# Kernel optimization log

Hardware: AMD Instinct MI355X
Metric: run time of the kernel (lower is better)

## Reference

```python
import jax, jax.numpy as jnp
import numpy as np

N, IN_FEATURES, OUT_FEATURES = 1048576, 32, 128


def setup_inputs() -> dict:
    key = jax.random.key(0)
    kx, kc = jax.random.split(key)
    x = jax.random.normal(kx, (N, IN_FEATURES), dtype=jnp.float32)
    # nn.init.normal_(centres, 0, 1); nn.init.constant_(log_sigmas, 0)
    centres = jax.random.normal(kc, (OUT_FEATURES, IN_FEATURES), dtype=jnp.float32)
    log_sigmas = jnp.zeros((OUT_FEATURES,), dtype=jnp.float32)
    return {"x": x, "centres": centres, "log_sigmas": log_sigmas}


def reference(x, centres, log_sigmas):
    x2 = jnp.sum(x * x, axis=-1, keepdims=True)            # (N, 1)
    c2 = jnp.sum(centres * centres, axis=-1)               # (out,)
    cross = jnp.einsum('ni,oi->no', x, centres)            # (N, out) GEMM
    sqdist = jnp.maximum(x2 - 2.0 * cross + c2, 0.0)       # clamp fp round-off
    # original: exp(-(sqrt(sqdist)/sigma)^2) == exp(-sqdist / sigma^2)
    inv_var = jnp.exp(-2.0 * log_sigmas)                   # (out,)
    return jnp.exp(-sqdist * inv_var)                      # (N, out)
```

## Files before the change

kernel.cpp:

```cpp
#include <hip/hip_runtime.h>

constexpr int IN_F   = 32;
constexpr int OUT_F  = 128;
constexpr int BLOCK  = 256;
constexpr int WAVES  = BLOCK / 64;
constexpr int RSTAGE = 8;

using f32x2  = __attribute__((ext_vector_type(2)))  float;
using f32x16 = __attribute__((ext_vector_type(16))) float;

__global__ __launch_bounds__(BLOCK, 4)
void rbf_kernel(const float* __restrict__ x,
                const float* __restrict__ centres,
                const float* __restrict__ log_sigmas,
                float* __restrict__ out,
                int rows_per_wave)
{
    __shared__ float4 xs[WAVES][RSTAGE][IN_F / 4];
    __shared__ float  x2s[WAVES][RSTAGE];

    const int tid  = threadIdx.x;
    const int wv   = tid >> 6;
    const int lane = tid & 63;

    const int o0 = lane * 2;
    const f32x16 c0lo = *reinterpret_cast<const f32x16*>(centres + (size_t)(o0 + 0) * IN_F);
    const f32x16 c0hi = *reinterpret_cast<const f32x16*>(centres + (size_t)(o0 + 0) * IN_F + 16);
    const f32x16 c1lo = *reinterpret_cast<const f32x16*>(centres + (size_t)(o0 + 1) * IN_F);
    const f32x16 c1hi = *reinterpret_cast<const f32x16*>(centres + (size_t)(o0 + 1) * IN_F + 16);

    float c2a = 0.f, c2b = 0.f;
    #pragma unroll
    for (int k = 0; k < 16; ++k) {
        c2a = fmaf(c0lo[k], c0lo[k], c2a);
        c2a = fmaf(c0hi[k], c0hi[k], c2a);
        c2b = fmaf(c1lo[k], c1lo[k], c2b);
        c2b = fmaf(c1hi[k], c1hi[k], c2b);
    }
    const float iv0 = __expf(-2.0f * log_sigmas[o0 + 0]);
    const float iv1 = __expf(-2.0f * log_sigmas[o0 + 1]);

    const size_t waveRow0 = ((size_t)blockIdx.x * WAVES + wv) * (size_t)rows_per_wave;
    const int rs = lane >> 3;
    const int q  = lane & 7;

    for (int it = 0; it < rows_per_wave; it += RSTAGE) {
        const float4 v = *reinterpret_cast<const float4*>(
            x + (waveRow0 + it) * IN_F + lane * 4);
        float s;
        s = v.x * v.x;
        s = fmaf(v.y, v.y, s);
        s = fmaf(v.z, v.z, s);
        s = fmaf(v.w, v.w, s);
        s += __shfl_xor(s, 1);
        s += __shfl_xor(s, 2);
        s += __shfl_xor(s, 4);
        xs[wv][rs][q] = v;
        if (q == 0) x2s[wv][rs] = s;
        __syncthreads();

        #pragma unroll
        for (int rr = 0; rr < RSTAGE; ++rr) {
            float acc0 = 0.f, acc1 = 0.f;
            #pragma unroll
            for (int u = 0; u < 4; ++u) {
                const float4 xq = xs[wv][rr][u];
                acc0 = fmaf(xq.x, c0lo[4*u+0], acc0);
                acc0 = fmaf(xq.y, c0lo[4*u+1], acc0);
                acc0 = fmaf(xq.z, c0lo[4*u+2], acc0);
                acc0 = fmaf(xq.w, c0lo[4*u+3], acc0);
                acc1 = fmaf(xq.x, c1lo[4*u+0], acc1);
                acc1 = fmaf(xq.y, c1lo[4*u+1], acc1);
                acc1 = fmaf(xq.z, c1lo[4*u+2], acc1);
                acc1 = fmaf(xq.w, c1lo[4*u+3], acc1);
            }
            #pragma unroll
            for (int u = 0; u < 4; ++u) {
                const float4 xq = xs[wv][rr][4 + u];
                acc0 = fmaf(xq.x, c0hi[4*u+0], acc0);
                acc0 = fmaf(xq.y, c0hi[4*u+1], acc0);
                acc0 = fmaf(xq.z, c0hi[4*u+2], acc0);
                acc0 = fmaf(xq.w, c0hi[4*u+3], acc0);
                acc1 = fmaf(xq.x, c1hi[4*u+0], acc1);
                acc1 = fmaf(xq.y, c1hi[4*u+1], acc1);
                acc1 = fmaf(xq.z, c1hi[4*u+2], acc1);
                acc1 = fmaf(xq.w, c1hi[4*u+3], acc1);
            }
            const float x2 = x2s[wv][rr];
            const float t0 = fmaxf(fmaf(-2.0f, acc0, x2 + c2a), 0.0f);
            const float t1 = fmaxf(fmaf(-2.0f, acc1, x2 + c2b), 0.0f);
            f32x2 o;
            o.x = __expf(-t0 * iv0);
            o.y = __expf(-t1 * iv1);
            __builtin_nontemporal_store(o,
                reinterpret_cast<f32x2*>(out + (waveRow0 + it + rr) * OUT_F + o0));
        }
        __syncthreads();
    }
}

extern "C" void kernel_launch(void* const* d_in, const int* in_sizes, int n_in,
                              void* d_out, int out_size, void* d_ws, size_t ws_size,
                              hipStream_t stream) {
    const float* x          = (const float*)d_in[0];
    const float* centres    = (const float*)d_in[1];
    const float* log_sigmas = (const float*)d_in[2];
    float* out = (float*)d_out;

    const int n = in_sizes[0] / IN_F;
    const int blocks = 2048;
    const int rows_per_block = n / blocks;
    const int rows_per_wave  = rows_per_block / WAVES;
    rbf_kernel<<<blocks, BLOCK, 0, stream>>>(x, centres, log_sigmas, out, rows_per_wave);
}
```

Before: 152.7 us.

## Split K across half-waves with permlane swap, packed FMA, and double-buffered staging

Each lane now computes four output columns over half of the input features, and partial sums from the two half-waves are combined with v_permlane32_swap. Dot products use packed two-wide FMAs, and outputs are written as float4 vectors. The x tile is staged in double-buffered LDS with a register prefetch two stages ahead, and block-wide barriers are replaced by a per-wave LDS waitcnt. The grid is doubled and output stores are no longer nontemporal, which could change cache behaviour on the large output write.

```diff
diff --git a/kernel.cpp b/kernel.cpp
--- a/kernel.cpp
+++ b/kernel.cpp
@@ -9,6 +9,10 @@
 using f32x2  = __attribute__((ext_vector_type(2)))  float;
 using f32x16 = __attribute__((ext_vector_type(16))) float;
 
+__device__ __forceinline__ void swap32(float& a, float& b) {
+    asm volatile("v_permlane32_swap_b32 %0, %1" : "+v"(a), "+v"(b));
+}
+
 __global__ __launch_bounds__(BLOCK, 4)
 void rbf_kernel(const float* __restrict__ x,
                 const float* __restrict__ centres,
@@ -16,86 +20,130 @@
                 float* __restrict__ out,
                 int rows_per_wave)
 {
-    __shared__ float4 xs[WAVES][RSTAGE][IN_F / 4];
-    __shared__ float  x2s[WAVES][RSTAGE];
+    __shared__ float4 xs[WAVES][2][RSTAGE][IN_F / 4];
+    __shared__ float  x2s[WAVES][2][RSTAGE];
 
     const int tid  = threadIdx.x;
     const int wv   = tid >> 6;
     const int lane = tid & 63;
+    const int j    = lane & 31;
+    const int h    = lane >> 5;
 
-    const int o0 = lane * 2;
-    const f32x16 c0lo = *reinterpret_cast<const f32x16*>(centres + (size_t)(o0 + 0) * IN_F);
-    const f32x16 c0hi = *reinterpret_cast<const f32x16*>(centres + (size_t)(o0 + 0) * IN_F + 16);
-    const f32x16 c1lo = *reinterpret_cast<const f32x16*>(centres + (size_t)(o0 + 1) * IN_F);
-    const f32x16 c1hi = *reinterpret_cast<const f32x16*>(centres + (size_t)(o0 + 1) * IN_F + 16);
+    const float* cb = centres + (size_t)(4 * j) * IN_F + 16 * h;
+    const f32x16 cA = *reinterpret_cast<const f32x16*>(cb + 0 * IN_F);
+    const f32x16 cB = *reinterpret_cast<const f32x16*>(cb + 1 * IN_F);
+    const f32x16 cC = *reinterpret_cast<const f32x16*>(cb + 2 * IN_F);
+    const f32x16 cD = *reinterpret_cast<const f32x16*>(cb + 3 * IN_F);
 
-    float c2a = 0.f, c2b = 0.f;
+    float q0 = 0.f, q1 = 0.f, q2 = 0.f, q3 = 0.f;
     #pragma unroll
     for (int k = 0; k < 16; ++k) {
-        c2a = fmaf(c0lo[k], c0lo[k], c2a);
-        c2a = fmaf(c0hi[k], c0hi[k], c2a);
-        c2b = fmaf(c1lo[k], c1lo[k], c2b);
-        c2b = fmaf(c1hi[k], c1hi[k], c2b);
+        q0 = fmaf(cA[k], cA[k], q0);
+        q1 = fmaf(cB[k], cB[k], q1);
+        q2 = fmaf(cC[k], cC[k], q2);
+        q3 = fmaf(cD[k], cD[k], q3);
     }
-    const float iv0 = __expf(-2.0f * log_sigmas[o0 + 0]);
-    const float iv1 = __expf(-2.0f * log_sigmas[o0 + 1]);
+    float ta, tb;
+    ta = q0; tb = q0; swap32(ta, tb); const float c20 = ta + tb;
+    ta = q1; tb = q1; swap32(ta, tb); const float c21 = ta + tb;
+    ta = q2; tb = q2; swap32(ta, tb); const float c22 = ta + tb;
+    ta = q3; tb = q3; swap32(ta, tb); const float c23 = ta + tb;
+
+    const float4 ls4 = *reinterpret_cast<const float4*>(log_sigmas + 4 * j);
+    const float iv0 = __expf(-2.0f * ls4.x);
+    const float iv1 = __expf(-2.0f * ls4.y);
+    const float iv2 = __expf(-2.0f * ls4.z);
+    const float iv3 = __expf(-2.0f * ls4.w);
 
     const size_t waveRow0 = ((size_t)blockIdx.x * WAVES + wv) * (size_t)rows_per_wave;
+    const float* xb = x   + waveRow0 * IN_F;
+    float*       ob = out + waveRow0 * OUT_F + 4 * j;
+
     const int rs = lane >> 3;
     const int q  = lane & 7;
+    const int nst = rows_per_wave / RSTAGE;
 
-    for (int it = 0; it < rows_per_wave; it += RSTAGE) {
-        const float4 v = *reinterpret_cast<const float4*>(
-            x + (waveRow0 + it) * IN_F + lane * 4);
-        float s;
-        s = v.x * v.x;
-        s = fmaf(v.y, v.y, s);
-        s = fmaf(v.z, v.z, s);
-        s = fmaf(v.w, v.w, s);
-        s += __shfl_xor(s, 1);
-        s += __shfl_xor(s, 2);
-        s += __shfl_xor(s, 4);
-        xs[wv][rs][q] = v;
-        if (q == 0) x2s[wv][rs] = s;
-        __syncthreads();
+    float4 vcur = *reinterpret_cast<const float4*>(xb + (size_t)rs * IN_F + q * 4);
+    float4 vnxt = *reinterpret_cast<const float4*>(xb + (size_t)(RSTAGE + rs) * IN_F + q * 4);
 
+    for (int s = 0; s < nst; ++s) {
+        const int buf = s & 1;
+
+        float ss = vcur.x * vcur.x;
+        ss = fmaf(vcur.y, vcur.y, ss);
+        ss = fmaf(vcur.z, vcur.z, ss);
+        ss = fmaf(vcur.w, vcur.w, ss);
+        ss += __shfl_xor(ss, 1);
+        ss += __shfl_xor(ss, 2);
+        ss += __shfl_xor(ss, 4);
+        xs[wv][buf][rs][q] = vcur;
+        if (q == 0) x2s[wv][buf][rs] = ss;
+        asm volatile("s_waitcnt lgkmcnt(0)" ::: "memory");
+        __builtin_amdgcn_sched_barrier(0);
+
+        vcur = vnxt;
+        if (s + 2 < nst)
+            vnxt = *reinterpret_cast<const float4*>(
+                xb + (size_t)((s + 2) * RSTAGE + rs) * IN_F + q * 4);
+
+        float4 rr[4];
         #pragma unroll
-        for (int rr = 0; rr < RSTAGE; ++rr) {
-            float acc0 = 0.f, acc1 = 0.f;
+        for (int m = 0; m < 4; ++m) {
+            f32x2 pA0 = {0.f,0.f}, pA1 = {0.f,0.f}, pA2 = {0.f,0.f}, pA3 = {0.f,0.f};
+            f32x2 pB0 = {0.f,0.f}, pB1 = {0.f,0.f}, pB2 = {0.f,0.f}, pB3 = {0.f,0.f};
             #pragma unroll
             for (int u = 0; u < 4; ++u) {
-                const float4 xq = xs[wv][rr][u];
-                acc0 = fmaf(xq.x, c0lo[4*u+0], acc0);
-                acc0 = fmaf(xq.y, c0lo[4*u+1], acc0);
-                acc0 = fmaf(xq.z, c0lo[4*u+2], acc0);
-                acc0 = fmaf(xq.w, c0lo[4*u+3], acc0);
-                acc1 = fmaf(xq.x, c1lo[4*u+0], acc1);
-                acc1 = fmaf(xq.y, c1lo[4*u+1], acc1);
-                acc1 = fmaf(xq.z, c1lo[4*u+2], acc1);
-                acc1 = fmaf(xq.w, c1lo[4*u+3], acc1);
+                const float4 xa = xs[wv][buf][2*m + 0][h * 4 + u];
+                const float4 xv = xs[wv][buf][2*m + 1][h * 4 + u];
+                const f32x2 ea0 = {xa.x, xa.y}, ea1 = {xa.z, xa.w};
+                const f32x2 eb0 = {xv.x, xv.y}, eb1 = {xv.z, xv.w};
+                const f32x2 cA0 = {cA[4*u+0], cA[4*u+1]}, cA1 = {cA[4*u+2], cA[4*u+3]};
+                const f32x2 cB0 = {cB[4*u+0], cB[4*u+1]}, cB1 = {cB[4*u+2], cB[4*u+3]};
+                const f32x2 cC0 = {cC[4*u+0], cC[4*u+1]}, cC1 = {cC[4*u+2], cC[4*u+3]};
+                const f32x2 cD0 = {cD[4*u+0], cD[4*u+1]}, cD1 = {cD[4*u+2], cD[4*u+3]};
+                pA0 = __builtin_elementwise_fma(ea0, cA0, pA0);
+                pA0 = __builtin_elementwise_fma(ea1, cA1, pA0);
+                pA1 = __builtin_elementwise_fma(ea0, cB0, pA1);
+                pA1 = __builtin_elementwise_fma(ea1, cB1, pA1);
+                pA2 = __builtin_elementwise_fma(ea0, cC0, pA2);
+                pA2 = __builtin_elementwise_fma(ea1, cC1, pA2);
+                pA3 = __builtin_elementwise_fma(ea0, cD0, pA3);
+                pA3 = __builtin_elementwise_fma(ea1, cD1, pA3);
+                pB0 = __builtin_elementwise_fma(eb0, cA0, pB0);
+                pB0 = __builtin_elementwise_fma(eb1, cA1, pB0);
+                pB1 = __builtin_elementwise_fma(eb0, cB0, pB1);
+                pB1 = __builtin_elementwise_fma(eb1, cB1, pB1);
+                pB2 = __builtin_elementwise_fma(eb0, cC0, pB2);
+                pB2 = __builtin_elementwise_fma(eb1, cC1, pB2);
+                pB3 = __builtin_elementwise_fma(eb0, cD0, pB3);
+                pB3 = __builtin_elementwise_fma(eb1, cD1, pB3);
             }
-            #pragma unroll
-            for (int u = 0; u < 4; ++u) {
-                const float4 xq = xs[wv][rr][4 + u];
-                acc0 = fmaf(xq.x, c0hi[4*u+0], acc0);
-                acc0 = fmaf(xq.y, c0hi[4*u+1], acc0);
-                acc0 = fmaf(xq.z, c0hi[4*u+2], acc0);
-                acc0 = fmaf(xq.w, c0hi[4*u+3], acc0);
-                acc1 = fmaf(xq.x, c1hi[4*u+0], acc1);
-                acc1 = fmaf(xq.y, c1hi[4*u+1], acc1);
-                acc1 = fmaf(xq.z, c1hi[4*u+2], acc1);
-                acc1 = fmaf(xq.w, c1hi[4*u+3], acc1);
-            }
-            const float x2 = x2s[wv][rr];
-            const float t0 = fmaxf(fmaf(-2.0f, acc0, x2 + c2a), 0.0f);
-            const float t1 = fmaxf(fmaf(-2.0f, acc1, x2 + c2b), 0.0f);
-            f32x2 o;
-            o.x = __expf(-t0 * iv0);
-            o.y = __expf(-t1 * iv1);
-            __builtin_nontemporal_store(o,
-                reinterpret_cast<f32x2*>(out + (waveRow0 + it + rr) * OUT_F + o0));
+            float sA0 = pA0.x + pA0.y, sB0 = pB0.x + pB0.y;
+            float sA1 = pA1.x + pA1.y, sB1 = pB1.x + pB1.y;
+            float sA2 = pA2.x + pA2.y, sB2 = pB2.x + pB2.y;
+            float sA3 = pA3.x + pA3.y, sB3 = pB3.x + pB3.y;
+            swap32(sA0, sB0); const float d0 = sA0 + sB0;
+            swap32(sA1, sB1); const float d1 = sA1 + sB1;
+            swap32(sA2, sB2); const float d2 = sA2 + sB2;
+            swap32(sA3, sB3); const float d3 = sA3 + sB3;
+
+            const float x2v = x2s[wv][buf][2*m + h];
+            const float t0 = fmaxf(fmaf(-2.0f, d0, x2v + c20), 0.0f);
+            const float t1 = fmaxf(fmaf(-2.0f, d1, x2v + c21), 0.0f);
+            const float t2 = fmaxf(fmaf(-2.0f, d2, x2v + c22), 0.0f);
+            const float t3 = fmaxf(fmaf(-2.0f, d3, x2v + c23), 0.0f);
+            float4 o4;
+            o4.x = __expf(-t0 * iv0);
+            o4.y = __expf(-t1 * iv1);
+            o4.z = __expf(-t2 * iv2);
+            o4.w = __expf(-t3 * iv3);
+            rr[m] = o4;
         }
-        __syncthreads();
+
+        float* os = ob + (size_t)(s * RSTAGE + h) * OUT_F;
+        #pragma unroll
+        for (int m = 0; m < 4; ++m)
+            *reinterpret_cast<float4*>(os + (size_t)(2 * m) * OUT_F) = rr[m];
     }
 }
 
@@ -108,8 +156,7 @@
     float* out = (float*)d_out;
 
     const int n = in_sizes[0] / IN_F;
-    const int blocks = 2048;
-    const int rows_per_block = n / blocks;
-    const int rows_per_wave  = rows_per_block / WAVES;
+    const int blocks = 4096;
+    const int rows_per_wave = n / (blocks * WAVES);
     rbf_kernel<<<blocks, BLOCK, 0, stream>>>(x, centres, log_sigmas, out, rows_per_wave);
 }
```

After: 374.4 us. 2.45x slower.
